# Performance work log

Measured on AMD Instinct MI355X. Metric: run time of the kernel, lower is better.

Reference implementation:

```python
import jax, jax.numpy as jnp
import numpy as np

N_NODES = 50000
N_EDGES = 800000
D = 64
L = 2


def setup_inputs() -> dict:
    key = jax.random.key(0)
    ks = jax.random.split(key, 5)
    h = jax.random.normal(ks[0], (N_NODES, D), dtype=jnp.float32)
    Ws = jax.random.normal(ks[1], (L, D, D), dtype=jnp.float32) / np.sqrt(D)
    bs = jnp.zeros((L, D), dtype=jnp.float32)
    edge_weight = jax.random.uniform(ks[2], (N_EDGES,), dtype=jnp.float32)
    src = jax.random.randint(ks[3], (N_EDGES,), 0, N_NODES, dtype=jnp.int64)
    dst = jax.random.randint(ks[4], (N_EDGES,), 0, N_NODES, dtype=jnp.int64)
    return {"h": h, "Ws": Ws, "bs": bs, "edge_weight": edge_weight, "src": src, "dst": dst}


def reference(h, Ws, bs, edge_weight, src, dst):
    # DGL GraphConv(norm='none', activation=relu) with in_feats==out_feats:
    # aggregate-then-transform: agg[v] = sum_{e:(u->v)} w_e * h[u]; h' = relu(agg @ W + b)
    n = h.shape[0]
    for l in range(Ws.shape[0]):
        msg = h[src] * edge_weight[:, None]                      # [E, D] gather + scale
        agg = jax.ops.segment_sum(msg, dst, num_segments=n)      # [N, D] scatter-add
        h = jax.nn.relu(agg @ Ws[l] + bs[l])
    return h
```

## Files before the change

### kernel.cpp

```cpp
#include <hip/hip_runtime.h>
#include <hip/hip_fp16.h>

#define NN 50000
#define NE 800000
#define DD 64
#define BS 64
#define NB 782
#define ECAP 1280
#define CHUNK 3200
#define NPB 250
#define NITEMS (NN * DD / 8)

typedef __attribute__((ext_vector_type(8))) short short8;
typedef __attribute__((ext_vector_type(4))) float f32x4;

__device__ __forceinline__ unsigned packh2(float lo, float hi) {
    __half2 h = __floats2half2_rn(lo, hi);
    return *reinterpret_cast<unsigned*>(&h);
}

__global__ __launch_bounds__(256) void f32_to_f16_zero_kernel(
        const float4* __restrict__ in4, uint4* __restrict__ out4,
        int* __restrict__ gpos, const float* __restrict__ Ws,
        uint4* __restrict__ wfrag) {
    if (blockIdx.x == 0) {
        for (int j = threadIdx.x; j < NB; j += 256) gpos[j] = 0;
    }
    if (blockIdx.x == 1 || blockIdx.x == 2) {
        int L = blockIdx.x - 1;
        const float* W = Ws + L * DD * DD;
        for (int e = threadIdx.x; e < 512; e += 256) {
            int w = e >> 7, s = (e >> 6) & 1, l = e & 63;
            int col = w * 16 + (l & 15);
            int k0 = 32 * s + 8 * (l >> 4);
            uint4 u;
            unsigned* up = (unsigned*)&u;
            #pragma unroll
            for (int uu = 0; uu < 4; ++uu)
                up[uu] = packh2(W[(k0 + 2 * uu) * DD + col],
                                W[(k0 + 2 * uu + 1) * DD + col]);
            wfrag[L * 512 + e] = u;
        }
    }
    int i = blockIdx.x * blockDim.x + threadIdx.x;
    if (i >= NITEMS) return;
    float4 a = in4[2 * i], b = in4[2 * i + 1];
    uint4 o;
    o.x = packh2(a.x, a.y); o.y = packh2(a.z, a.w);
    o.z = packh2(b.x, b.y); o.w = packh2(b.z, b.w);
    out4[i] = o;
}

__global__ __launch_bounds__(1024) void partition_kernel(
        const int* __restrict__ src, const int* __restrict__ dst,
        const float* __restrict__ ew,
        int* __restrict__ gpos, uint2* __restrict__ ebuf) {
    __shared__ int hist[NB];
    __shared__ int base[NB];
    int t = threadIdx.x;
    int c0 = blockIdx.x * CHUNK;
    for (int j = t; j < NB; j += 1024) hist[j] = 0;
    __syncthreads();
    short rank[4];
    int dcache[4];
    #pragma unroll
    for (int i = 0; i < 4; ++i) {
        int o = i * 1024 + t;
        if (o < CHUNK) {
            int d = dst[c0 + o];
            dcache[i] = d;
            rank[i] = (short)atomicAdd(&hist[d >> 6], 1);
        }
    }
    __syncthreads();
    for (int j = t; j < NB; j += 1024) {
        int c = hist[j];
        base[j] = c ? atomicAdd(&gpos[j], c) : 0;
    }
    __syncthreads();
    #pragma unroll
    for (int i = 0; i < 4; ++i) {
        int o = i * 1024 + t;
        if (o < CHUNK) {
            int e = c0 + o;
            int d = dcache[i];
            int bkt = d >> 6;
            int dl = d & 63;
            int pos = base[bkt] + (int)rank[i];
            if (pos < ECAP) {
                ebuf[(size_t)bkt * ECAP + pos] =
                    make_uint2((unsigned)src[e] | ((unsigned)dl << 16),
                               __float_as_uint(ew[e]));
            }
        }
    }
}

__global__ __launch_bounds__(512, 6) void sort_layer0_kernel(
        const uint2* __restrict__ ebuf, const int* __restrict__ gpos,
        const uint2* __restrict__ hh,
        const uint4* __restrict__ wfrag,
        const float* __restrict__ bvec,
        unsigned* __restrict__ sorted, int4* __restrict__ nodespan,
        void* __restrict__ h1out) {
    __shared__ unsigned led[ECAP];
    __shared__ int hist[BS], sc[BS];
    __shared__ int dh[128], dsc[128];
    __shared__ int4 nsp[BS];
    __shared__ unsigned Ahf[BS * 36];
    __shared__ float Dls[BS * 68];
    int t = threadIdx.x;
    int b = blockIdx.x;
    int cnt = min(gpos[b], ECAP);
    const uint2* slab = ebuf + (size_t)b * ECAP;

    if (t < BS) hist[t] = 0;
    if (t < 128) dh[t] = 0;
    __syncthreads();

    unsigned pay[3];
    int dl[3], rk[3];
    #pragma unroll
    for (int i = 0; i < 3; ++i) {
        int o = i * 512 + t;
        if (o < cnt) {
            uint2 q = slab[o];
            dl[i] = (int)(q.x >> 16);
            unsigned w16 = (unsigned)__half_as_ushort(
                __float2half(__uint_as_float(q.y)));
            pay[i] = (q.x & 0xFFFFu) | (w16 << 16);
            rk[i] = atomicAdd(&hist[dl[i]], 1);
        }
    }
    __syncthreads();
    if (t < BS) sc[t] = hist[t];
    __syncthreads();
    #pragma unroll
    for (int off = 1; off < BS; off <<= 1) {
        int v = (t < BS && t >= off) ? sc[t - off] : 0;
        __syncthreads();
        if (t < BS) sc[t] += v;
        __syncthreads();
    }
    unsigned* oslab = sorted + (size_t)b * ECAP;
    #pragma unroll
    for (int i = 0; i < 3; ++i) {
        int o = i * 512 + t;
        if (o < cnt) {
            int pos = sc[dl[i]] - hist[dl[i]] + rk[i];
            led[pos] = pay[i];
            oslab[pos] = pay[i];
        }
    }
    int nn_b = min(BS, NN - b * BS);
    if (t < nn_b) atomicAdd(&dh[min(hist[t], 127)], 1);
    __syncthreads();
    if (t < 128) dsc[t] = dh[t];
    __syncthreads();
    #pragma unroll
    for (int off = 1; off < 128; off <<= 1) {
        int v = (t < 128 && t >= off) ? dsc[t - off] : 0;
        __syncthreads();
        if (t < 128) dsc[t] += v;
        __syncthreads();
    }
    if (t < 128) dh[t] = dsc[t] - dh[t];
    __syncthreads();
    if (t < nn_b) {
        int d = min(hist[t], 127);
        int p = atomicAdd(&dh[d], 1);
        nsp[p] = make_int4(sc[t] - hist[t], hist[t], b * BS + t, 0);
        nodespan[b * BS + p] =
            make_int4(b * ECAP + sc[t] - hist[t], hist[t], b * BS + t, 0);
    } else if (t < BS) {
        nsp[t] = make_int4(0, 0, NN, 0);
        nodespan[b * BS + t] = make_int4(0, 0, NN, 0);
    }
    __syncthreads();

    int lane = t & 15;
    unsigned ul = (unsigned)lane;
    __half2 z = __floats2half2_rn(0.f, 0.f);
    #pragma unroll
    for (int pass = 0; pass < 2; ++pass) {
        int g = (t >> 4) + pass * 32;
        int4 sp = nsp[g];
        const unsigned* lrow = led + sp.x;
        int deg = sp.y;
        __half2 a0 = z, a1 = z, b0 = z, b1 = z, c0 = z, c1 = z, d0 = z, d1 = z;
        int j = 0;
        for (; j + 4 <= deg; j += 4) {
            unsigned q0 = lrow[j + 0], q1 = lrow[j + 1];
            unsigned q2 = lrow[j + 2], q3 = lrow[j + 3];
            uint2 r0 = hh[(q0 & 0xFFFFu) * 16u + ul];
            uint2 r1 = hh[(q1 & 0xFFFFu) * 16u + ul];
            uint2 r2 = hh[(q2 & 0xFFFFu) * 16u + ul];
            uint2 r3 = hh[(q3 & 0xFFFFu) * 16u + ul];
            __half2 w0 = __half2half2(__ushort_as_half((unsigned short)(q0 >> 16)));
            __half2 w1 = __half2half2(__ushort_as_half((unsigned short)(q1 >> 16)));
            __half2 w2 = __half2half2(__ushort_as_half((unsigned short)(q2 >> 16)));
            __half2 w3 = __half2half2(__ushort_as_half((unsigned short)(q3 >> 16)));
            a0 = __hfma2(w0, *(const __half2*)&r0.x, a0);
            a1 = __hfma2(w0, *(const __half2*)&r0.y, a1);
            b0 = __hfma2(w1, *(const __half2*)&r1.x, b0);
            b1 = __hfma2(w1, *(const __half2*)&r1.y, b1);
            c0 = __hfma2(w2, *(const __half2*)&r2.x, c0);
            c1 = __hfma2(w2, *(const __half2*)&r2.y, c1);
            d0 = __hfma2(w3, *(const __half2*)&r3.x, d0);
            d1 = __hfma2(w3, *(const __half2*)&r3.y, d1);
        }
        for (; j < deg; ++j) {
            unsigned q0 = lrow[j];
            uint2 r0 = hh[(q0 & 0xFFFFu) * 16u + ul];
            __half2 w0 = __half2half2(__ushort_as_half((unsigned short)(q0 >> 16)));
            a0 = __hfma2(w0, *(const __half2*)&r0.x, a0);
            a1 = __hfma2(w0, *(const __half2*)&r0.y, a1);
        }
        a0 = __hadd2(__hadd2(a0, b0), __hadd2(c0, d0));
        a1 = __hadd2(__hadd2(a1, b1), __hadd2(c1, d1));
        Ahf[g * 36 + 2 * lane]     = *reinterpret_cast<unsigned*>(&a0);
        Ahf[g * 36 + 2 * lane + 1] = *reinterpret_cast<unsigned*>(&a1);
    }
    __syncthreads();

    {
        int w = t >> 6;
        int l = t & 63;
        #pragma unroll
        for (int i = 0; i < 2; ++i) {
            int T = w + 8 * i;
            int rt = T >> 2, ct = T & 3;
            const uint4* arow = (const uint4*)&Ahf[(rt * 16 + (l & 15)) * 36];
            uint4 au0 = arow[l >> 4];
            uint4 au1 = arow[4 + (l >> 4)];
            uint4 bu0 = wfrag[(ct * 2 + 0) * 64 + l];
            uint4 bu1 = wfrag[(ct * 2 + 1) * 64 + l];
            f32x4 d = {0.f, 0.f, 0.f, 0.f};
            d = __builtin_amdgcn_mfma_f32_16x16x32_f16(
                    *(const short8*)&au0, *(const short8*)&bu0, d, 0, 0, 0);
            d = __builtin_amdgcn_mfma_f32_16x16x32_f16(
                    *(const short8*)&au1, *(const short8*)&bu1, d, 0, 0, 0);
            #pragma unroll
            for (int r = 0; r < 4; ++r)
                Dls[(rt * 16 + (l >> 4) * 4 + r) * 68 + ct * 16 + (l & 15)] = d[r];
        }
    }
    __syncthreads();

    #pragma unroll
    for (int i = 0; i < 2; ++i) {
        int idx = i * 512 + t;
        int g2 = idx >> 4, ln = idx & 15;
        float4 bias = reinterpret_cast<const float4*>(bvec)[ln];
        float4 dv = *reinterpret_cast<const float4*>(&Dls[g2 * 68 + ln * 4]);
        float4 o;
        o.x = fmaxf(dv.x + bias.x, 0.f);
        o.y = fmaxf(dv.y + bias.y, 0.f);
        o.z = fmaxf(dv.z + bias.z, 0.f);
        o.w = fmaxf(dv.w + bias.w, 0.f);
        int node = nsp[g2].z;
        if (node < NN) {
            reinterpret_cast<uint2*>(h1out)[(size_t)node * 16 + ln] =
                make_uint2(packh2(o.x, o.y), packh2(o.z, o.w));
        }
    }
}

__global__ __launch_bounds__(256) void gcn_layer1_kernel(
        const uint2* __restrict__ hh,
        const unsigned* __restrict__ sorted,
        const int4* __restrict__ nodespan,
        const uint4* __restrict__ wfrag,
        const float* __restrict__ bvec,
        float4* __restrict__ outp) {
    __shared__ unsigned Ahf[16 * 36];
    __shared__ float Dls[16 * 68];
    __shared__ int nid[16];
    int t = threadIdx.x;
    int g = t >> 4;
    int lane = t & 15;
    int v = blockIdx.x * 16 + g;

    int4 sp = nodespan[v];
    if (lane == 0) nid[g] = sp.z;
    const unsigned* row = sorted + sp.x;
    int deg = sp.y;

    __half2 z = __floats2half2_rn(0.f, 0.f);
    __half2 a0 = z, a1 = z, b0 = z, b1 = z, c0 = z, c1 = z, d0 = z, d1 = z;
    unsigned ul = (unsigned)lane;
    for (int k0 = 0; k0 < deg; k0 += 16) {
        int kk = k0 + lane;
        unsigned q = (kk < deg) ? row[kk] : 0u;
        int lim = min(16, deg - k0);
        int j = 0;
        for (; j + 4 <= lim; j += 4) {
            unsigned q0 = (unsigned)__shfl((int)q, j + 0, 16);
            unsigned q1 = (unsigned)__shfl((int)q, j + 1, 16);
            unsigned q2 = (unsigned)__shfl((int)q, j + 2, 16);
            unsigned q3 = (unsigned)__shfl((int)q, j + 3, 16);
            uint2 r0 = hh[(q0 & 0xFFFFu) * 16u + ul];
            uint2 r1 = hh[(q1 & 0xFFFFu) * 16u + ul];
            uint2 r2 = hh[(q2 & 0xFFFFu) * 16u + ul];
            uint2 r3 = hh[(q3 & 0xFFFFu) * 16u + ul];
            __half2 w0 = __half2half2(__ushort_as_half((unsigned short)(q0 >> 16)));
            __half2 w1 = __half2half2(__ushort_as_half((unsigned short)(q1 >> 16)));
            __half2 w2 = __half2half2(__ushort_as_half((unsigned short)(q2 >> 16)));
            __half2 w3 = __half2half2(__ushort_as_half((unsigned short)(q3 >> 16)));
            a0 = __hfma2(w0, *(const __half2*)&r0.x, a0);
            a1 = __hfma2(w0, *(const __half2*)&r0.y, a1);
            b0 = __hfma2(w1, *(const __half2*)&r1.x, b0);
            b1 = __hfma2(w1, *(const __half2*)&r1.y, b1);
            c0 = __hfma2(w2, *(const __half2*)&r2.x, c0);
            c1 = __hfma2(w2, *(const __half2*)&r2.y, c1);
            d0 = __hfma2(w3, *(const __half2*)&r3.x, d0);
            d1 = __hfma2(w3, *(const __half2*)&r3.y, d1);
        }
        for (; j < lim; ++j) {
            unsigned q0 = (unsigned)__shfl((int)q, j, 16);
            uint2 r0 = hh[(q0 & 0xFFFFu) * 16u + ul];
            __half2 w0 = __half2half2(__ushort_as_half((unsigned short)(q0 >> 16)));
            a0 = __hfma2(w0, *(const __half2*)&r0.x, a0);
            a1 = __hfma2(w0, *(const __half2*)&r0.y, a1);
        }
    }
    a0 = __hadd2(__hadd2(a0, b0), __hadd2(c0, d0));
    a1 = __hadd2(__hadd2(a1, b1), __hadd2(c1, d1));
    Ahf[g * 36 + 2 * lane]     = *reinterpret_cast<unsigned*>(&a0);
    Ahf[g * 36 + 2 * lane + 1] = *reinterpret_cast<unsigned*>(&a1);
    __syncthreads();

    {
        int w = t >> 6;
        int l = t & 63;
        const uint4* arow = (const uint4*)(&Ahf[(l & 15) * 36]);
        uint4 au0 = arow[l >> 4];
        uint4 au1 = arow[4 + (l >> 4)];
        uint4 bu0 = wfrag[(w * 2 + 0) * 64 + l];
        uint4 bu1 = wfrag[(w * 2 + 1) * 64 + l];
        f32x4 d = {0.f, 0.f, 0.f, 0.f};
        d = __builtin_amdgcn_mfma_f32_16x16x32_f16(
                *(const short8*)&au0, *(const short8*)&bu0, d, 0, 0, 0);
        d = __builtin_amdgcn_mfma_f32_16x16x32_f16(
                *(const short8*)&au1, *(const short8*)&bu1, d, 0, 0, 0);
        #pragma unroll
        for (int r = 0; r < 4; ++r)
            Dls[((l >> 4) * 4 + r) * 68 + w * 16 + (l & 15)] = d[r];
    }
    __syncthreads();

    float4 bias = reinterpret_cast<const float4*>(bvec)[lane];
    float4 dv = *reinterpret_cast<const float4*>(&Dls[g * 68 + lane * 4]);
    float4 o;
    o.x = fmaxf(dv.x + bias.x, 0.f);
    o.y = fmaxf(dv.y + bias.y, 0.f);
    o.z = fmaxf(dv.z + bias.z, 0.f);
    o.w = fmaxf(dv.w + bias.w, 0.f);
    int node = nid[g];
    if (node < NN) outp[(size_t)node * 16 + lane] = o;
}

extern "C" void kernel_launch(void* const* d_in, const int* in_sizes, int n_in,
                              void* d_out, int out_size, void* d_ws, size_t ws_size,
                              hipStream_t stream) {
    const float4* h4  = (const float4*)d_in[0];
    const float*  Ws  = (const float*)d_in[1];
    const float*  bsv = (const float*)d_in[2];
    const float*  ew  = (const float*)d_in[3];
    const int*    src = (const int*)d_in[4];
    const int*    dst = (const int*)d_in[5];
    float4* out = (float4*)d_out;
    char* ws = (char*)d_ws;

    int*      gpos     = (int*)(ws);
    uint2*    ebuf     = (uint2*)(ws + 64 * 1024);
    unsigned* sorted   = (unsigned*)(ws + 9u * 1024 * 1024);
    uint4*    wfrag    = (uint4*)(ws + 13u * 1024 * 1024);
    int4*     nodespan = (int4*)(ws + 13u * 1024 * 1024 + 256 * 1024);
    uint2*    h_hf     = (uint2*)(ws + 14u * 1024 * 1024 + 512 * 1024);
    void*     h1       = (void*)(ws + 24u * 1024 * 1024);

    f32_to_f16_zero_kernel<<<(NITEMS + 255) / 256, 256, 0, stream>>>(
        h4, (uint4*)h_hf, gpos, Ws, wfrag);
    partition_kernel<<<NPB, 1024, 0, stream>>>(src, dst, ew, gpos, ebuf);
    sort_layer0_kernel<<<NB, 512, 0, stream>>>(
        ebuf, gpos, h_hf, wfrag, bsv, sorted, nodespan, h1);
    gcn_layer1_kernel<<<NN / 16, 256, 0, stream>>>(
        (const uint2*)h1, sorted, nodespan, wfrag + 512, bsv + DD, out);
}
```

Baseline: 60.55 us.

## Restructure layer-1 kernel into per-bucket blocks staging edge lists in LDS

The layer-1 kernel now runs one 512-thread block per 64-node bucket instead of one 256-thread block per 16 nodes. Each block loads its bucket's sorted edge slab into shared memory and reads edge entries from LDS, where before it loaded them per 16-edge chunk and broadcast them with shuffles. The MFMA transform covers a 64x64 tile per block across 8 waves, mirroring the layer-0 kernel. This cuts the block count and the per-node shuffle overhead but reduces block-level parallelism. It also drops the occupancy hint on the layer-0 kernel and fixes empty nodespan offsets so they point at the bucket base.

```diff
diff --git a/kernel.cpp b/kernel.cpp
--- a/kernel.cpp
+++ b/kernel.cpp
@@ -96,7 +96,7 @@
     }
 }
 
-__global__ __launch_bounds__(512, 6) void sort_layer0_kernel(
+__global__ __launch_bounds__(512) void sort_layer0_kernel(
         const uint2* __restrict__ ebuf, const int* __restrict__ gpos,
         const uint2* __restrict__ hh,
         const uint4* __restrict__ wfrag,
@@ -174,7 +174,7 @@
             make_int4(b * ECAP + sc[t] - hist[t], hist[t], b * BS + t, 0);
     } else if (t < BS) {
         nsp[t] = make_int4(0, 0, NN, 0);
-        nodespan[b * BS + t] = make_int4(0, 0, NN, 0);
+        nodespan[b * BS + t] = make_int4(b * ECAP, 0, NN, 0);
     }
     __syncthreads();
 
@@ -266,39 +266,49 @@
     }
 }
 
-__global__ __launch_bounds__(256) void gcn_layer1_kernel(
+__global__ __launch_bounds__(512) void gcn_layer1_kernel(
         const uint2* __restrict__ hh,
         const unsigned* __restrict__ sorted,
+        const int* __restrict__ gpos,
         const int4* __restrict__ nodespan,
         const uint4* __restrict__ wfrag,
         const float* __restrict__ bvec,
         float4* __restrict__ outp) {
-    __shared__ unsigned Ahf[16 * 36];
-    __shared__ float Dls[16 * 68];
-    __shared__ int nid[16];
+    __shared__ unsigned led[ECAP];
+    __shared__ int4 nsp[BS];
+    __shared__ unsigned Ahf[BS * 36];
+    __shared__ float Dls[BS * 68];
     int t = threadIdx.x;
-    int g = t >> 4;
+    int b = blockIdx.x;
+    int cnt = min(gpos[b], ECAP);
+    const unsigned* slab = sorted + (size_t)b * ECAP;
+
+    #pragma unroll
+    for (int i = 0; i < 3; ++i) {
+        int o = i * 512 + t;
+        if (o < cnt) led[o] = slab[o];
+    }
+    if (t < BS) {
+        int4 sp = nodespan[b * BS + t];
+        sp.x -= b * ECAP;
+        nsp[t] = sp;
+    }
+    __syncthreads();
+
     int lane = t & 15;
-    int v = blockIdx.x * 16 + g;
-
-    int4 sp = nodespan[v];
-    if (lane == 0) nid[g] = sp.z;
-    const unsigned* row = sorted + sp.x;
-    int deg = sp.y;
-
+    unsigned ul = (unsigned)lane;
     __half2 z = __floats2half2_rn(0.f, 0.f);
-    __half2 a0 = z, a1 = z, b0 = z, b1 = z, c0 = z, c1 = z, d0 = z, d1 = z;
-    unsigned ul = (unsigned)lane;
-    for (int k0 = 0; k0 < deg; k0 += 16) {
-        int kk = k0 + lane;
-        unsigned q = (kk < deg) ? row[kk] : 0u;
-        int lim = min(16, deg - k0);
+    #pragma unroll
+    for (int pass = 0; pass < 2; ++pass) {
+        int g = (t >> 4) + pass * 32;
+        int4 sp = nsp[g];
+        const unsigned* lrow = led + sp.x;
+        int deg = sp.y;
+        __half2 a0 = z, a1 = z, b0 = z, b1 = z, c0 = z, c1 = z, d0 = z, d1 = z;
         int j = 0;
-        for (; j + 4 <= lim; j += 4) {
-            unsigned q0 = (unsigned)__shfl((int)q, j + 0, 16);
-            unsigned q1 = (unsigned)__shfl((int)q, j + 1, 16);
-            unsigned q2 = (unsigned)__shfl((int)q, j + 2, 16);
-            unsigned q3 = (unsigned)__shfl((int)q, j + 3, 16);
+        for (; j + 4 <= deg; j += 4) {
+            unsigned q0 = lrow[j + 0], q1 = lrow[j + 1];
+            unsigned q2 = lrow[j + 2], q3 = lrow[j + 3];
             uint2 r0 = hh[(q0 & 0xFFFFu) * 16u + ul];
             uint2 r1 = hh[(q1 & 0xFFFFu) * 16u + ul];
             uint2 r2 = hh[(q2 & 0xFFFFu) * 16u + ul];
@@ -316,48 +326,58 @@
             d0 = __hfma2(w3, *(const __half2*)&r3.x, d0);
             d1 = __hfma2(w3, *(const __half2*)&r3.y, d1);
         }
-        for (; j < lim; ++j) {
-            unsigned q0 = (unsigned)__shfl((int)q, j, 16);
+        for (; j < deg; ++j) {
+            unsigned q0 = lrow[j];
             uint2 r0 = hh[(q0 & 0xFFFFu) * 16u + ul];
             __half2 w0 = __half2half2(__ushort_as_half((unsigned short)(q0 >> 16)));
             a0 = __hfma2(w0, *(const __half2*)&r0.x, a0);
             a1 = __hfma2(w0, *(const __half2*)&r0.y, a1);
         }
-    }
-    a0 = __hadd2(__hadd2(a0, b0), __hadd2(c0, d0));
-    a1 = __hadd2(__hadd2(a1, b1), __hadd2(c1, d1));
-    Ahf[g * 36 + 2 * lane]     = *reinterpret_cast<unsigned*>(&a0);
-    Ahf[g * 36 + 2 * lane + 1] = *reinterpret_cast<unsigned*>(&a1);
+        a0 = __hadd2(__hadd2(a0, b0), __hadd2(c0, d0));
+        a1 = __hadd2(__hadd2(a1, b1), __hadd2(c1, d1));
+        Ahf[g * 36 + 2 * lane]     = *reinterpret_cast<unsigned*>(&a0);
+        Ahf[g * 36 + 2 * lane + 1] = *reinterpret_cast<unsigned*>(&a1);
+    }
     __syncthreads();
 
     {
         int w = t >> 6;
         int l = t & 63;
-        const uint4* arow = (const uint4*)(&Ahf[(l & 15) * 36]);
-        uint4 au0 = arow[l >> 4];
-        uint4 au1 = arow[4 + (l >> 4)];
-        uint4 bu0 = wfrag[(w * 2 + 0) * 64 + l];
-        uint4 bu1 = wfrag[(w * 2 + 1) * 64 + l];
-        f32x4 d = {0.f, 0.f, 0.f, 0.f};
-        d = __builtin_amdgcn_mfma_f32_16x16x32_f16(
-                *(const short8*)&au0, *(const short8*)&bu0, d, 0, 0, 0);
-        d = __builtin_amdgcn_mfma_f32_16x16x32_f16(
-                *(const short8*)&au1, *(const short8*)&bu1, d, 0, 0, 0);
         #pragma unroll
-        for (int r = 0; r < 4; ++r)
-            Dls[((l >> 4) * 4 + r) * 68 + w * 16 + (l & 15)] = d[r];
-    }
-    __syncthreads();
-
-    float4 bias = reinterpret_cast<const float4*>(bvec)[lane];
-    float4 dv = *reinterpret_cast<const float4*>(&Dls[g * 68 + lane * 4]);
-    float4 o;
-    o.x = fmaxf(dv.x + bias.x, 0.f);
-    o.y = fmaxf(dv.y + bias.y, 0.f);
-    o.z = fmaxf(dv.z + bias.z, 0.f);
-    o.w = fmaxf(dv.w + bias.w, 0.f);
-    int node = nid[g];
-    if (node < NN) outp[(size_t)node * 16 + lane] = o;
+        for (int i = 0; i < 2; ++i) {
+            int T = w + 8 * i;
+            int rt = T >> 2, ct = T & 3;
+            const uint4* arow = (const uint4*)&Ahf[(rt * 16 + (l & 15)) * 36];
+            uint4 au0 = arow[l >> 4];
+            uint4 au1 = arow[4 + (l >> 4)];
+            uint4 bu0 = wfrag[(ct * 2 + 0) * 64 + l];
+            uint4 bu1 = wfrag[(ct * 2 + 1) * 64 + l];
+            f32x4 d = {0.f, 0.f, 0.f, 0.f};
+            d = __builtin_amdgcn_mfma_f32_16x16x32_f16(
+                    *(const short8*)&au0, *(const short8*)&bu0, d, 0, 0, 0);
+            d = __builtin_amdgcn_mfma_f32_16x16x32_f16(
+                    *(const short8*)&au1, *(const short8*)&bu1, d, 0, 0, 0);
+            #pragma unroll
+            for (int r = 0; r < 4; ++r)
+                Dls[(rt * 16 + (l >> 4) * 4 + r) * 68 + ct * 16 + (l & 15)] = d[r];
+        }
+    }
+    __syncthreads();
+
+    #pragma unroll
+    for (int i = 0; i < 2; ++i) {
+        int idx = i * 512 + t;
+        int g2 = idx >> 4, ln = idx & 15;
+        float4 bias = reinterpret_cast<const float4*>(bvec)[ln];
+        float4 dv = *reinterpret_cast<const float4*>(&Dls[g2 * 68 + ln * 4]);
+        float4 o;
+        o.x = fmaxf(dv.x + bias.x, 0.f);
+        o.y = fmaxf(dv.y + bias.y, 0.f);
+        o.z = fmaxf(dv.z + bias.z, 0.f);
+        o.w = fmaxf(dv.w + bias.w, 0.f);
+        int node = nsp[g2].z;
+        if (node < NN) outp[(size_t)node * 16 + ln] = o;
+    }
 }
 
 extern "C" void kernel_launch(void* const* d_in, const int* in_sizes, int n_in,
@@ -385,6 +405,6 @@
     partition_kernel<<<NPB, 1024, 0, stream>>>(src, dst, ew, gpos, ebuf);
     sort_layer0_kernel<<<NB, 512, 0, stream>>>(
         ebuf, gpos, h_hf, wfrag, bsv, sorted, nodespan, h1);
-    gcn_layer1_kernel<<<NN / 16, 256, 0, stream>>>(
-        (const uint2*)h1, sorted, nodespan, wfrag + 512, bsv + DD, out);
-}
+    gcn_layer1_kernel<<<NB, 512, 0, stream>>>(
+        (const uint2*)h1, sorted, gpos, nodespan, wfrag + 512, bsv + DD, out);
+}
```

Result: no change. 59.99 us (-0.9%).
